# Optimization experiments

Hardware: AMD Instinct MI355X
Metric: run time of the kernel (lower is better)

## Reference

```python
import jax, jax.numpy as jnp
import numpy as np

THRESHOLD = 0.2
MARGIN = 2
TEMP = 0.1


def _margin_mask(h0, w0, h1, w1):
    # interior-valid mask per spatial dim (margin_remove=b removed on both ends;
    # mask0 is None so h0s=h0 etc. and the symmetric trailing-b removal applies)
    def interior(n):
        i = jnp.arange(n)
        return (i >= MARGIN) & (i < n - MARGIN)
    m = (interior(h0)[:, None, None, None]
         & interior(w0)[None, :, None, None]
         & interior(h1)[None, None, :, None]
         & interior(w1)[None, None, None, :])  # [h0,w0,h1,w1]
    return m.reshape(1, h0 * w0, h1 * w1)


def setup_inputs() -> dict:
    key = jax.random.key(0)
    k0, k1 = jax.random.split(key)
    x0 = jax.random.normal(k0, (1, 6400, 256), dtype=jnp.float32)
    x1 = jax.random.normal(k1, (1, 6400, 256), dtype=jnp.float32)
    return {"x0": x0, "x1": x1, "h0": 80, "w0": 80, "h1": 80, "w1": 80}


def reference(x0, x1, h0, w0, h1, w1):
    n, l, c = x0.shape
    s = x1.shape[1]
    # similarities = einsum / c / temp
    sim = jnp.einsum('nlc,nsc->nls', x0, x1) / (c * TEMP)
    # dual softmax confidences
    conf = jax.nn.softmax(sim, axis=2) * jax.nn.softmax(sim, axis=1)
    # threshold + margin removal (mask0=None branch of _remove_mask_margin)
    mask = (conf > THRESHOLD) & _margin_mask(h0, w0, h1, w1)
    # mutual top-1 (argmax via equality with row/col max, exactly as torch)
    m0 = conf == jnp.max(conf, axis=2, keepdims=True)
    m1 = conf == jnp.max(conf, axis=1, keepdims=True)
    mask = mask & m0 & m1
    # fixed-shape encoding of the match extraction: nonzero(mask) <=> nonzero of
    # this masked confidence map; matched confidences are its nonzero values.
    return conf * mask.astype(conf.dtype)
```

## Files before the change

kernel.cpp:

```cpp
#include <hip/hip_runtime.h>

namespace {

constexpr int Ldim = 6400;
constexpr int Sdim = 6400;
constexpr float INV_CT = 0.0390625f;
constexpr float THR = 0.2f;
constexpr int CAP = 65536;

typedef __attribute__((ext_vector_type(8))) short short8;
typedef __attribute__((ext_vector_type(4))) float f32x4;

__device__ __forceinline__ void atomicMaxPosF(float* addr, float v) {
  atomicMax(reinterpret_cast<unsigned int*>(addr), __float_as_uint(v));
}

__device__ __forceinline__ bool valid80(int idx) {
  const int i = idx / 80;
  const int j = idx - i * 80;
  return (i >= 2) & (i < 78) & (j >= 2) & (j < 78);
}

__device__ __forceinline__ unsigned short f2bf(float v) {
  unsigned u = __float_as_uint(v);
  return (unsigned short)((u + 0x7fffu + ((u >> 16) & 1u)) >> 16);
}

__device__ __forceinline__ float conf1(float s, float rs, float cs) {
  return expf(2.f * s) / (rs * cs);
}
__device__ __forceinline__ bool precand(float s, float lc, float cu) {
  return 2.f * s - lc > cu;
}

typedef const __attribute__((address_space(1))) unsigned int guint;
typedef __attribute__((address_space(3))) unsigned int suint;
__device__ __forceinline__ void gload16(const void* g, void* l) {
  __builtin_amdgcn_global_load_lds((guint*)g, (suint*)l, 16, 0, 0);
}


__global__ __launch_bounds__(256)
void k_split(const float* __restrict__ X, unsigned short* __restrict__ Xh) {
  const int g = blockIdx.x * 256 + threadIdx.x;
  const int r = g >> 5;
  const int gt = g & 31;
  const float* src = X + ((size_t)r << 8) + (gt << 3);
  const float4 a = *reinterpret_cast<const float4*>(src);
  const float4 b = *reinterpret_cast<const float4*>(src + 4);
  short8 hv;
  hv[0] = (short)f2bf(a.x); hv[1] = (short)f2bf(a.y);
  hv[2] = (short)f2bf(a.z); hv[3] = (short)f2bf(a.w);
  hv[4] = (short)f2bf(b.x); hv[5] = (short)f2bf(b.y);
  hv[6] = (short)f2bf(b.z); hv[7] = (short)f2bf(b.w);
  const int gp = (gt & 3) ^ ((r >> 1) & 3);
  const size_t dst = ((size_t)((gt >> 2) * Ldim + r) * 4 + gp) << 3;
  *reinterpret_cast<short8*>(Xh + dst) = hv;
}

__device__ __forceinline__ void gemm128(
    const unsigned short* __restrict__ A, const unsigned short* __restrict__ B,
    int m0, int n0, int wave, int lane,
    unsigned short (*sA)[4096], unsigned short (*sB)[4096], f32x4 acc[4][4]) {
  const int wr = wave >> 1, wc = wave & 1;
  const int ll = lane & 15;
  const int lg = lane >> 4;
  const int arow = lane >> 2;
  const int gsel = (lane & 3) * 8;

#pragma unroll
  for (int mi = 0; mi < 4; ++mi)
#pragma unroll
    for (int ni = 0; ni < 4; ++ni) acc[mi][ni] = (f32x4){0.f, 0.f, 0.f, 0.f};

  auto stage = [&](int slot, int ks) {
    const size_t kb = (size_t)ks * Ldim * 32;
#pragma unroll
    for (int p = 0; p < 2; ++p) {
      const int ch = wave * 2 + p;
      const size_t asrc = kb + (size_t)(m0 + ch * 16 + arow) * 32 + gsel;
      const size_t bsrc = kb + (size_t)(n0 + ch * 16 + arow) * 32 + gsel;
      gload16(A + asrc, &sA[slot][ch * 512]);
      gload16(B + bsrc, &sB[slot][ch * 512]);
    }
  };

  stage(0, 0);
  __syncthreads();

  for (int ks = 0; ks < 8; ++ks) {
    const int cur = ks & 1;
    if (ks < 7) stage(cur ^ 1, ks + 1);

    auto rd = [&](unsigned short* S, int row) -> short8 {
      const int gp = lg ^ ((row >> 1) & 3);
      return *reinterpret_cast<const short8*>(&S[(row * 4 + gp) * 8]);
    };
    short8 af[4], bfv[4];
#pragma unroll
    for (int mi = 0; mi < 4; ++mi) af[mi] = rd(sA[cur], wr * 64 + mi * 16 + ll);
#pragma unroll
    for (int ni = 0; ni < 4; ++ni) bfv[ni] = rd(sB[cur], wc * 64 + ni * 16 + ll);
#pragma unroll
    for (int mi = 0; mi < 4; ++mi)
#pragma unroll
      for (int ni = 0; ni < 4; ++ni)
        acc[mi][ni] = __builtin_amdgcn_mfma_f32_16x16x32_bf16(af[mi], bfv[ni], acc[mi][ni], 0, 0, 0);

    __syncthreads();
  }

#pragma unroll
  for (int mi = 0; mi < 4; ++mi)
#pragma unroll
    for (int ni = 0; ni < 4; ++ni) acc[mi][ni] *= INV_CT;
}

__global__ __launch_bounds__(256)
void k_gemm_stats(const unsigned short* __restrict__ A, const unsigned short* __restrict__ B,
                  float* __restrict__ Rsum, float* __restrict__ Csum) {
  __shared__ unsigned short sA[2][4096], sB[2][4096];
  const int tid = threadIdx.x;
  const int lane = tid & 63, wave = tid >> 6;
  const int bx = blockIdx.x % (Sdim / 128);
  const int by = blockIdx.x / (Sdim / 128);
  const int m0 = by * 128, n0 = bx * 128;
  const int wr = wave >> 1, wc = wave & 1;
  const int ll = lane & 15, lg = lane >> 4;

  f32x4 acc[4][4];
  gemm128(A, B, m0, n0, wave, lane, sA, sB, acc);

  float colp[4] = {0.f, 0.f, 0.f, 0.f};
#pragma unroll
  for (int mi = 0; mi < 4; ++mi)
#pragma unroll
    for (int r = 0; r < 4; ++r) {
      float re = 0.f;
#pragma unroll
      for (int ni = 0; ni < 4; ++ni) {
        const float e = expf(acc[mi][ni][r]);
        re += e;
        colp[ni] += e;
      }
      re += __shfl_xor(re, 1);
      re += __shfl_xor(re, 2);
      re += __shfl_xor(re, 4);
      re += __shfl_xor(re, 8);
      if (ll == 0)
        atomicAdd(&Rsum[m0 + wr * 64 + mi * 16 + lg * 4 + r], re);
    }
#pragma unroll
  for (int ni = 0; ni < 4; ++ni) {
    float c = colp[ni];
    c += __shfl_xor(c, 16);
    c += __shfl_xor(c, 32);
    if (lane < 16) atomicAdd(&Csum[n0 + wc * 64 + ni * 16 + lane], c);
  }
}

__global__ __launch_bounds__(256)
void k_logs(const float* __restrict__ Rsum, const float* __restrict__ Csum,
            float* __restrict__ lnC, float* __restrict__ cut) {
  const int i = blockIdx.x * 256 + threadIdx.x;
  lnC[i] = logf(Csum[i]);
  cut[i] = logf(Rsum[i]) + logf(THR) - 0.05f;
}

__global__ __launch_bounds__(256)
void k_gemm_cand(const unsigned short* __restrict__ A, const unsigned short* __restrict__ B,
                 const float* __restrict__ Rsum, const float* __restrict__ Csum,
                 const float* __restrict__ lnC, const float* __restrict__ cut,
                 float* __restrict__ RM, float* __restrict__ CM,
                 unsigned int* __restrict__ cnt, unsigned int* __restrict__ cidx,
                 float* __restrict__ cconf) {
  __shared__ unsigned short sA[2][4096], sB[2][4096];
  const int tid = threadIdx.x;
  const int lane = tid & 63, wave = tid >> 6;
  const int bx = blockIdx.x % (Sdim / 128);
  const int by = blockIdx.x / (Sdim / 128);
  const int m0 = by * 128, n0 = bx * 128;
  const int wr = wave >> 1, wc = wave & 1;
  const int ll = lane & 15, lg = lane >> 4;

  f32x4 acc[4][4];
  gemm128(A, B, m0, n0, wave, lane, sA, sB, acc);

  float lc[4];
#pragma unroll
  for (int ni = 0; ni < 4; ++ni) lc[ni] = lnC[n0 + wc * 64 + ni * 16 + ll];

#pragma unroll
  for (int mi = 0; mi < 4; ++mi)
#pragma unroll
    for (int r = 0; r < 4; ++r) {
      const int row = m0 + wr * 64 + mi * 16 + lg * 4 + r;
      const float cu = cut[row];
      const bool b0 = precand(acc[mi][0][r], lc[0], cu);
      const bool b1 = precand(acc[mi][1][r], lc[1], cu);
      const bool b2 = precand(acc[mi][2][r], lc[2], cu);
      const bool b3 = precand(acc[mi][3][r], lc[3], cu);
      if (b0 | b1 | b2 | b3) {
        const float rs = Rsum[row];
#pragma unroll
        for (int ni = 0; ni < 4; ++ni) {
          const bool b = (ni == 0) ? b0 : (ni == 1) ? b1 : (ni == 2) ? b2 : b3;
          if (b) {
            const int col = n0 + wc * 64 + ni * 16 + ll;
            const float c = conf1(acc[mi][ni][r], rs, Csum[col]);
            atomicMaxPosF(&RM[row], c);
            atomicMaxPosF(&CM[col], c);
            const unsigned t = atomicAdd(cnt, 1u);
            if (t < CAP) {
              cidx[t] = (unsigned)row * Sdim + col;
              cconf[t] = c;
            }
          }
        }
      }
    }
}

__global__ __launch_bounds__(256)
void k_scatter(const unsigned int* __restrict__ cnt, const unsigned int* __restrict__ cidx,
               const float* __restrict__ cconf, const float* __restrict__ RM,
               const float* __restrict__ CM, float* __restrict__ out) {
  const int n = (int)min(*cnt, (unsigned)CAP);
  for (int i = blockIdx.x * 256 + threadIdx.x; i < n; i += gridDim.x * 256) {
    const unsigned idx = cidx[i];
    const int l = idx / Sdim;
    const int s = idx - l * Sdim;
    const float c = cconf[i];
    if (c > THR && valid80(l) && valid80(s) && c == RM[l] && c == CM[s])
      out[idx] = c;
  }
}

}

extern "C" void kernel_launch(void* const* d_in, const int* in_sizes, int n_in,
                              void* d_out, int out_size, void* d_ws, size_t ws_size,
                              hipStream_t stream) {
  (void)in_sizes; (void)n_in; (void)out_size; (void)ws_size;
  const float* x0 = reinterpret_cast<const float*>(d_in[0]);
  const float* x1 = reinterpret_cast<const float*>(d_in[1]);
  float* out = reinterpret_cast<float*>(d_out);

  float* Rsum = reinterpret_cast<float*>(d_ws);
  float* Csum = Rsum + Ldim;
  float* RM = Csum + Sdim;
  float* CM = RM + Ldim;
  unsigned int* cnt = reinterpret_cast<unsigned int*>(CM + Sdim);
  float* lnC = reinterpret_cast<float*>(cnt + 4);
  float* cut = lnC + Sdim;
  unsigned int* cidx = reinterpret_cast<unsigned int*>(cut + Ldim);
  float* cconf = reinterpret_cast<float*>(cidx + CAP);
  unsigned short* XA = reinterpret_cast<unsigned short*>(cconf + CAP);
  const size_t PSZ = (size_t)8 * Ldim * 32;
  unsigned short* XB = XA + PSZ;

  hipMemsetAsync(d_ws, 0, sizeof(float) * (size_t)(4 * Ldim) + 16, stream);

  k_split<<<Ldim * 32 / 256, 256, 0, stream>>>(x0, XA);
  k_split<<<Ldim * 32 / 256, 256, 0, stream>>>(x1, XB);
  k_gemm_stats<<<(Ldim / 128) * (Sdim / 128), 256, 0, stream>>>(XA, XB, Rsum, Csum);
  k_logs<<<Ldim / 256, 256, 0, stream>>>(Rsum, Csum, lnC, cut);
  k_gemm_cand<<<(Ldim / 128) * (Sdim / 128), 256, 0, stream>>>(
      XA, XB, Rsum, Csum, lnC, cut, RM, CM, cnt, cidx, cconf);
  hipMemsetAsync(out, 0, sizeof(float) * (size_t)Ldim * Sdim, stream);
  k_scatter<<<64, 256, 0, stream>>>(cnt, cidx, cconf, RM, CM, out);
}
```

Before: 283.6 us.

## Fuse two GEMM passes into one using tile-local softmax bounds for candidates

Measured after the change: 274.7 us. -3.1%, faster.

```diff
diff --git a/kernel.cpp b/kernel.cpp
--- a/kernel.cpp
+++ b/kernel.cpp
@@ -28,9 +28,6 @@
 
 __device__ __forceinline__ float conf1(float s, float rs, float cs) {
   return expf(2.f * s) / (rs * cs);
-}
-__device__ __forceinline__ bool precand(float s, float lc, float cu) {
-  return 2.f * s - lc > cu;
 }
 
 typedef const __attribute__((address_space(1))) unsigned int guint;
@@ -74,7 +71,7 @@
     for (int ni = 0; ni < 4; ++ni) acc[mi][ni] = (f32x4){0.f, 0.f, 0.f, 0.f};
 
   auto stage = [&](int slot, int ks) {
-    const size_t kb = (size_t)ks * Ldim * 32;
+    const size_t kb = (size_t)ks * (Ldim * 32);
 #pragma unroll
     for (int p = 0; p < 2; ++p) {
       const int ch = wave * 2 + p;
@@ -117,104 +114,71 @@
 }
 
 __global__ __launch_bounds__(256)
-void k_gemm_stats(const unsigned short* __restrict__ A, const unsigned short* __restrict__ B,
-                  float* __restrict__ Rsum, float* __restrict__ Csum) {
+void k_gemm_all(const unsigned short* __restrict__ A, const unsigned short* __restrict__ B,
+                float* __restrict__ Rsum, float* __restrict__ Csum,
+                unsigned int* __restrict__ cnt, unsigned int* __restrict__ cidx,
+                float* __restrict__ csim) {
   __shared__ unsigned short sA[2][4096], sB[2][4096];
   const int tid = threadIdx.x;
   const int lane = tid & 63, wave = tid >> 6;
+  const int wr = wave >> 1, wc = wave & 1;
+  const int ll = lane & 15, lg = lane >> 4;
   const int bx = blockIdx.x % (Sdim / 128);
   const int by = blockIdx.x / (Sdim / 128);
   const int m0 = by * 128, n0 = bx * 128;
-  const int wr = wave >> 1, wc = wave & 1;
-  const int ll = lane & 15, lg = lane >> 4;
 
   f32x4 acc[4][4];
   gemm128(A, B, m0, n0, wave, lane, sA, sB, acc);
 
+  float re[16];
   float colp[4] = {0.f, 0.f, 0.f, 0.f};
 #pragma unroll
   for (int mi = 0; mi < 4; ++mi)
 #pragma unroll
     for (int r = 0; r < 4; ++r) {
-      float re = 0.f;
+      float s = 0.f;
 #pragma unroll
       for (int ni = 0; ni < 4; ++ni) {
         const float e = expf(acc[mi][ni][r]);
-        re += e;
+        s += e;
         colp[ni] += e;
       }
-      re += __shfl_xor(re, 1);
-      re += __shfl_xor(re, 2);
-      re += __shfl_xor(re, 4);
-      re += __shfl_xor(re, 8);
+      s += __shfl_xor(s, 1);
+      s += __shfl_xor(s, 2);
+      s += __shfl_xor(s, 4);
+      s += __shfl_xor(s, 8);
+      re[mi * 4 + r] = s;
       if (ll == 0)
-        atomicAdd(&Rsum[m0 + wr * 64 + mi * 16 + lg * 4 + r], re);
+        atomicAdd(&Rsum[m0 + wr * 64 + mi * 16 + lg * 4 + r], s);
     }
+  float clw[4];
 #pragma unroll
   for (int ni = 0; ni < 4; ++ni) {
     float c = colp[ni];
     c += __shfl_xor(c, 16);
     c += __shfl_xor(c, 32);
+    clw[ni] = c;
     if (lane < 16) atomicAdd(&Csum[n0 + wc * 64 + ni * 16 + lane], c);
   }
-}
-
-__global__ __launch_bounds__(256)
-void k_logs(const float* __restrict__ Rsum, const float* __restrict__ Csum,
-            float* __restrict__ lnC, float* __restrict__ cut) {
-  const int i = blockIdx.x * 256 + threadIdx.x;
-  lnC[i] = logf(Csum[i]);
-  cut[i] = logf(Rsum[i]) + logf(THR) - 0.05f;
-}
-
-__global__ __launch_bounds__(256)
-void k_gemm_cand(const unsigned short* __restrict__ A, const unsigned short* __restrict__ B,
-                 const float* __restrict__ Rsum, const float* __restrict__ Csum,
-                 const float* __restrict__ lnC, const float* __restrict__ cut,
-                 float* __restrict__ RM, float* __restrict__ CM,
-                 unsigned int* __restrict__ cnt, unsigned int* __restrict__ cidx,
-                 float* __restrict__ cconf) {
-  __shared__ unsigned short sA[2][4096], sB[2][4096];
-  const int tid = threadIdx.x;
-  const int lane = tid & 63, wave = tid >> 6;
-  const int bx = blockIdx.x % (Sdim / 128);
-  const int by = blockIdx.x / (Sdim / 128);
-  const int m0 = by * 128, n0 = bx * 128;
-  const int wr = wave >> 1, wc = wave & 1;
-  const int ll = lane & 15, lg = lane >> 4;
-
-  f32x4 acc[4][4];
-  gemm128(A, B, m0, n0, wave, lane, sA, sB, acc);
-
+
+  constexpr float L018 = -1.7147984f;
   float lc[4];
 #pragma unroll
-  for (int ni = 0; ni < 4; ++ni) lc[ni] = lnC[n0 + wc * 64 + ni * 16 + ll];
-
+  for (int ni = 0; ni < 4; ++ni) lc[ni] = 0.5f * logf(clw[ni]);
 #pragma unroll
   for (int mi = 0; mi < 4; ++mi)
 #pragma unroll
     for (int r = 0; r < 4; ++r) {
-      const int row = m0 + wr * 64 + mi * 16 + lg * 4 + r;
-      const float cu = cut[row];
-      const bool b0 = precand(acc[mi][0][r], lc[0], cu);
-      const bool b1 = precand(acc[mi][1][r], lc[1], cu);
-      const bool b2 = precand(acc[mi][2][r], lc[2], cu);
-      const bool b3 = precand(acc[mi][3][r], lc[3], cu);
-      if (b0 | b1 | b2 | b3) {
-        const float rs = Rsum[row];
-#pragma unroll
-        for (int ni = 0; ni < 4; ++ni) {
-          const bool b = (ni == 0) ? b0 : (ni == 1) ? b1 : (ni == 2) ? b2 : b3;
-          if (b) {
-            const int col = n0 + wc * 64 + ni * 16 + ll;
-            const float c = conf1(acc[mi][ni][r], rs, Csum[col]);
-            atomicMaxPosF(&RM[row], c);
-            atomicMaxPosF(&CM[col], c);
-            const unsigned t = atomicAdd(cnt, 1u);
-            if (t < CAP) {
-              cidx[t] = (unsigned)row * Sdim + col;
-              cconf[t] = c;
-            }
+      const float tr = 0.5f * (L018 + logf(re[mi * 4 + r]));
+#pragma unroll
+      for (int ni = 0; ni < 4; ++ni) {
+        if (acc[mi][ni][r] > tr + lc[ni]) {
+          const int row = m0 + wr * 64 + mi * 16 + lg * 4 + r;
+          const int col = n0 + wc * 64 + ni * 16 + ll;
+          const unsigned t = atomicAdd(cnt, 1u);
+          if (t < CAP) {
+            cidx[t] = (unsigned)row * Sdim + col;
+            csim[t] = acc[mi][ni][r];
           }
         }
       }
@@ -222,9 +186,26 @@
 }
 
 __global__ __launch_bounds__(256)
-void k_scatter(const unsigned int* __restrict__ cnt, const unsigned int* __restrict__ cidx,
-               const float* __restrict__ cconf, const float* __restrict__ RM,
-               const float* __restrict__ CM, float* __restrict__ out) {
+void k_final1(const unsigned int* __restrict__ cnt, const unsigned int* __restrict__ cidx,
+              const float* __restrict__ csim, const float* __restrict__ Rsum,
+              const float* __restrict__ Csum, float* __restrict__ RM,
+              float* __restrict__ CM, float* __restrict__ cconf) {
+  const int n = (int)min(*cnt, (unsigned)CAP);
+  for (int i = blockIdx.x * 256 + threadIdx.x; i < n; i += gridDim.x * 256) {
+    const unsigned idx = cidx[i];
+    const int l = idx / Sdim;
+    const int s = idx - l * Sdim;
+    const float c = conf1(csim[i], Rsum[l], Csum[s]);
+    cconf[i] = c;
+    atomicMaxPosF(&RM[l], c);
+    atomicMaxPosF(&CM[s], c);
+  }
+}
+
+__global__ __launch_bounds__(256)
+void k_final2(const unsigned int* __restrict__ cnt, const unsigned int* __restrict__ cidx,
+              const float* __restrict__ cconf, const float* __restrict__ RM,
+              const float* __restrict__ CM, float* __restrict__ out) {
   const int n = (int)min(*cnt, (unsigned)CAP);
   for (int i = blockIdx.x * 256 + threadIdx.x; i < n; i += gridDim.x * 256) {
     const unsigned idx = cidx[i];
@@ -251,10 +232,9 @@
   float* RM = Csum + Sdim;
   float* CM = RM + Ldim;
   unsigned int* cnt = reinterpret_cast<unsigned int*>(CM + Sdim);
-  float* lnC = reinterpret_cast<float*>(cnt + 4);
-  float* cut = lnC + Sdim;
-  unsigned int* cidx = reinterpret_cast<unsigned int*>(cut + Ldim);
-  float* cconf = reinterpret_cast<float*>(cidx + CAP);
+  unsigned int* cidx = cnt + 4;
+  float* csim = reinterpret_cast<float*>(cidx + CAP);
+  float* cconf = csim + CAP;
   unsigned short* XA = reinterpret_cast<unsigned short*>(cconf + CAP);
   const size_t PSZ = (size_t)8 * Ldim * 32;
   unsigned short* XB = XA + PSZ;
@@ -263,10 +243,9 @@
 
   k_split<<<Ldim * 32 / 256, 256, 0, stream>>>(x0, XA);
   k_split<<<Ldim * 32 / 256, 256, 0, stream>>>(x1, XB);
-  k_gemm_stats<<<(Ldim / 128) * (Sdim / 128), 256, 0, stream>>>(XA, XB, Rsum, Csum);
-  k_logs<<<Ldim / 256, 256, 0, stream>>>(Rsum, Csum, lnC, cut);
-  k_gemm_cand<<<(Ldim / 128) * (Sdim / 128), 256, 0, stream>>>(
-      XA, XB, Rsum, Csum, lnC, cut, RM, CM, cnt, cidx, cconf);
+  k_gemm_all<<<(Ldim / 128) * (Sdim / 128), 256, 0, stream>>>(
+      XA, XB, Rsum, Csum, cnt, cidx, csim);
   hipMemsetAsync(out, 0, sizeof(float) * (size_t)Ldim * Sdim, stream);
-  k_scatter<<<64, 256, 0, stream>>>(cnt, cidx, cconf, RM, CM, out);
-}
+  k_final1<<<32, 256, 0, stream>>>(cnt, cidx, csim, Rsum, Csum, RM, CM, cconf);
+  k_final2<<<32, 256, 0, stream>>>(cnt, cidx, cconf, RM, CM, out);
+}
```
